# Kernel optimization log

Hardware: AMD Instinct MI355X
Metric: run time of the kernel (lower is better)

Reference implementation:

```python
import jax, jax.numpy as jnp
import numpy as np

B, L, Q, K, H = 64, 1024, 1024, 1024, 1024

def setup_inputs() -> dict:
    key = jax.random.key(0)
    k1, k2, k3, k4, k5, k6 = jax.random.split(key, 6)
    query = jax.random.normal(k1, (B, Q), dtype=jnp.float32)
    keys = jax.random.normal(k2, (B, L, K), dtype=jnp.float32)
    mask = jax.random.randint(k3, (B, L), 0, 2).astype(bool)
    # nn.Linear weights: W1 [H, Q], W2 [H, K], v [1, H], all bias-free
    W1 = jax.random.normal(k4, (H, Q), dtype=jnp.float32) / np.sqrt(Q)
    W2 = jax.random.normal(k5, (H, K), dtype=jnp.float32) / np.sqrt(K)
    v = jax.random.normal(k6, (1, H), dtype=jnp.float32) / np.sqrt(H)
    return {"query": query, "keys": keys, "mask": mask, "W1": W1, "W2": W2, "v": v}

def reference(query, keys, mask, W1, W2, v):
    # q: [B, H], broadcast over seq dim instead of expand
    q = query @ W1.T                                  # [B, H]
    k = jnp.einsum('blk,hk->blh', keys, W2)           # [B, L, H]
    scores = jnp.tanh(q[:, None, :] + k) @ v[0]       # [B, L]
    scores = jnp.where(mask, -jnp.inf, scores)
    weights = jax.nn.softmax(scores, axis=-1)
    weights = jnp.nan_to_num(weights, nan=0.0)
    context = jnp.einsum('bl,blk->bk', weights, keys) # [B, K]
    return (context, weights)
```

## Files before the change

kernel.cpp:

```cpp
#include <hip/hip_runtime.h>
#include <math.h>


typedef __attribute__((ext_vector_type(8))) short short8;
typedef __attribute__((ext_vector_type(4))) float floatx4;

__device__ __forceinline__ short f2bf(float x) {
    unsigned u = __float_as_uint(x);
    u += 0x7fffu + ((u >> 16) & 1u);
    return (short)(u >> 16);
}
__device__ __forceinline__ short8 pack8(float4 lo, float4 hi) {
    short8 r;
    r[0]=f2bf(lo.x); r[1]=f2bf(lo.y); r[2]=f2bf(lo.z); r[3]=f2bf(lo.w);
    r[4]=f2bf(hi.x); r[5]=f2bf(hi.y); r[6]=f2bf(hi.z); r[7]=f2bf(hi.w);
    return r;
}
__device__ __forceinline__ float fast_tanh(float x) {
    const float e = __expf(2.f * x);
    return 1.f - 2.f * __builtin_amdgcn_rcpf(e + 1.f);
}

#define LDA 40

__global__ __launch_bounds__(256) void k0_zero(float* __restrict__ out) {
    const int i = (blockIdx.x * 256 + threadIdx.x) * 4;
    const float4 z = {0.f, 0.f, 0.f, 0.f};
    *(float4*)(out + i) = z;
}

__global__ __launch_bounds__(256) void k1_qproj(
    const float* __restrict__ query, const float* __restrict__ W1,
    float* __restrict__ out)
{
    __shared__ float As[32][64];
    __shared__ float Bs[32][64];
    const int t  = threadIdx.x;
    const int tx = t & 15, ty = t >> 4;
    const int h0 = blockIdx.x * 64;
    const int kbase = blockIdx.y * 256;
    const int sr = t >> 2;
    const int sk = (t & 3) * 8;
    float c[4][4] = {{0.f}};
    for (int k0 = kbase; k0 < kbase + 256; k0 += 32) {
        const float4 a0 = *(const float4*)(query + sr * 1024 + k0 + sk);
        const float4 a1 = *(const float4*)(query + sr * 1024 + k0 + sk + 4);
        const float4 b0 = *(const float4*)(W1 + (h0 + sr) * 1024 + k0 + sk);
        const float4 b1 = *(const float4*)(W1 + (h0 + sr) * 1024 + k0 + sk + 4);
        __syncthreads();
        As[sk+0][sr]=a0.x; As[sk+1][sr]=a0.y; As[sk+2][sr]=a0.z; As[sk+3][sr]=a0.w;
        As[sk+4][sr]=a1.x; As[sk+5][sr]=a1.y; As[sk+6][sr]=a1.z; As[sk+7][sr]=a1.w;
        Bs[sk+0][sr]=b0.x; Bs[sk+1][sr]=b0.y; Bs[sk+2][sr]=b0.z; Bs[sk+3][sr]=b0.w;
        Bs[sk+4][sr]=b1.x; Bs[sk+5][sr]=b1.y; Bs[sk+6][sr]=b1.z; Bs[sk+7][sr]=b1.w;
        __syncthreads();
        #pragma unroll
        for (int k = 0; k < 32; ++k) {
            const float4 av = *(const float4*)&As[k][ty*4];
            const float4 bv = *(const float4*)&Bs[k][tx*4];
            const float aa[4] = {av.x, av.y, av.z, av.w};
            const float bb[4] = {bv.x, bv.y, bv.z, bv.w};
            #pragma unroll
            for (int i = 0; i < 4; ++i)
                #pragma unroll
                for (int j = 0; j < 4; ++j)
                    c[i][j] = fmaf(aa[i], bb[j], c[i][j]);
        }
    }
    #pragma unroll
    for (int i = 0; i < 4; ++i)
        #pragma unroll
        for (int j = 0; j < 4; ++j)
            atomicAdd(&out[(ty*4 + i) * 1024 + h0 + tx*4 + j], c[i][j]);
}

__global__ __launch_bounds__(256) void k_pack(const float* __restrict__ src,
                                              short* __restrict__ dst, int nunits)
{
    const int stride = gridDim.x * 256;
    for (int o = blockIdx.x * 256 + threadIdx.x; o < nunits; o += stride) {
        const int m = o & 15;
        const int c = (o >> 4) & 127;
        const int panel = o >> 11;
        const size_t f = ((size_t)panel * 16 + m) * 1024 + c * 8;
        const float4 a = *(const float4*)(src + f);
        const float4 b = *(const float4*)(src + f + 4);
        ((short8*)dst)[o] = pack8(a, b);
    }
}

__global__ __launch_bounds__(256) void k2_scores_full(
    const short* __restrict__ keysp, const short* __restrict__ W2p,
    const float* __restrict__ v, float* __restrict__ out)
{
    __shared__ float red[128][33];
    const int t  = threadIdx.x;
    const int l0 = blockIdx.x * 128;
    const int b  = blockIdx.y;
    const float* q = out;
    float* score = out + 65536;

    const int lane = t & 63, wid = t >> 6;
    const int quad = lane >> 4, m16 = lane & 15;
    const int wm = (wid >> 1) * 64;
    const int wn = (wid & 1) * 64;

    const short8* pA = (const short8*)keysp
        + ((size_t)(b * 64 + (l0 >> 4) + (wm >> 4))) * 2048 + quad * 16 + m16;

    float s_loc[4][4] = {{0.f}};

    for (int hb = 0; hb < 8; ++hb) {
        const short8* pB = (const short8*)W2p
            + ((size_t)(hb * 8 + (wn >> 4))) * 2048 + quad * 16 + m16;

        floatx4 acc[4][4] = {};
        short8 a0[4], b0[4], a1[4], b1[4];
        #pragma unroll
        for (int i = 0; i < 4; ++i) { a0[i] = pA[i * 2048]; b0[i] = pB[i * 2048]; }

        for (int kk = 0; kk < 928; kk += 64) {
            #pragma unroll
            for (int i = 0; i < 4; ++i) {
                a1[i] = pA[i * 2048 + (kk + 32) * 2];
                b1[i] = pB[i * 2048 + (kk + 32) * 2];
            }
            #pragma unroll
            for (int i = 0; i < 4; ++i)
                #pragma unroll
                for (int j = 0; j < 4; ++j)
                    acc[i][j] = __builtin_amdgcn_mfma_f32_16x16x32_bf16(a0[i], b0[j], acc[i][j], 0, 0, 0);
            #pragma unroll
            for (int i = 0; i < 4; ++i) {
                a0[i] = pA[i * 2048 + (kk + 64) * 2];
                b0[i] = pB[i * 2048 + (kk + 64) * 2];
            }
            #pragma unroll
            for (int i = 0; i < 4; ++i)
                #pragma unroll
                for (int j = 0; j < 4; ++j)
                    acc[i][j] = __builtin_amdgcn_mfma_f32_16x16x32_bf16(a1[i], b1[j], acc[i][j], 0, 0, 0);
        }
        #pragma unroll
        for (int i = 0; i < 4; ++i) {
            a1[i] = pA[i * 2048 + 992 * 2];
            b1[i] = pB[i * 2048 + 992 * 2];
        }
        #pragma unroll
        for (int i = 0; i < 4; ++i)
            #pragma unroll
            for (int j = 0; j < 4; ++j)
                acc[i][j] = __builtin_amdgcn_mfma_f32_16x16x32_bf16(a0[i], b0[j], acc[i][j], 0, 0, 0);
        #pragma unroll
        for (int i = 0; i < 4; ++i)
            #pragma unroll
            for (int j = 0; j < 4; ++j)
                acc[i][j] = __builtin_amdgcn_mfma_f32_16x16x32_bf16(a1[i], b1[j], acc[i][j], 0, 0, 0);

        float qv[4], vv[4];
        #pragma unroll
        for (int j = 0; j < 4; ++j) {
            const int h = hb * 128 + wn + j * 16 + m16;
            qv[j] = q[b * 1024 + h];
            vv[j] = v[h];
        }
        #pragma unroll
        for (int i = 0; i < 4; ++i)
            #pragma unroll
            for (int r = 0; r < 4; ++r) {
                float s = 0.f;
                #pragma unroll
                for (int j = 0; j < 4; ++j)
                    s += fast_tanh(qv[j] + acc[i][j][r]) * vv[j];
                s_loc[i][r] += s;
            }
    }

    #pragma unroll
    for (int i = 0; i < 4; ++i)
        #pragma unroll
        for (int r = 0; r < 4; ++r)
            red[wm + i * 16 + quad * 4 + r][(wid & 1) * 16 + m16] = s_loc[i][r];
    __syncthreads();
    if (t < 128) {
        const float* rr = red[t];
        float s = 0.f;
        #pragma unroll
        for (int c = 0; c < 32; ++c) s += rr[c];
        score[b * 1024 + l0 + t] = s;
    }
}

__global__ __launch_bounds__(256) void k2_scores(
    const float* __restrict__ keys, const float* __restrict__ W2,
    const float* __restrict__ v, float* __restrict__ out)
{
    __shared__ union {
        struct { short A[128][LDA]; short B[128][LDA]; } st;
        float red[128][33];
    } sm;
    const int t  = threadIdx.x;
    const int hb = blockIdx.x;
    const int l0 = blockIdx.y * 128;
    const int b  = blockIdx.z;
    const int h0 = hb * 128;
    const float* q = out;
    float* score = out + 65536;

    const int srow = t >> 1;
    const int skh  = (t & 1) * 16;
    const float* Arow = keys + ((size_t)(b * 1024 + l0 + srow)) * 1024 + skh;
    const float* Brow = W2   + ((size_t)(h0 + srow)) * 1024 + skh;

    const int lane = t & 63, wid = t >> 6;
    const int quad = lane >> 4, m16 = lane & 15;
    const int wm = (wid >> 1) * 64;
    const int wn = (wid & 1) * 64;

    floatx4 acc[4][4] = {};

    for (int kk = 0; kk < 1024; kk += 32) {
        const float4 a0 = *(const float4*)(Arow + kk);
        const float4 a1 = *(const float4*)(Arow + kk + 4);
        const float4 a2 = *(const float4*)(Arow + kk + 8);
        const float4 a3 = *(const float4*)(Arow + kk + 12);
        const float4 w0 = *(const float4*)(Brow + kk);
        const float4 w1 = *(const float4*)(Brow + kk + 4);
        const float4 w2 = *(const float4*)(Brow + kk + 8);
        const float4 w3 = *(const float4*)(Brow + kk + 12);
        __syncthreads();
        *(short8*)&sm.st.A[srow][skh]     = pack8(a0, a1);
        *(short8*)&sm.st.A[srow][skh + 8] = pack8(a2, a3);
        *(short8*)&sm.st.B[srow][skh]     = pack8(w0, w1);
        *(short8*)&sm.st.B[srow][skh + 8] = pack8(w2, w3);
        __syncthreads();
        short8 af[4], bf[4];
        #pragma unroll
        for (int i = 0; i < 4; ++i)
            af[i] = *(const short8*)&sm.st.A[wm + i*16 + m16][quad * 8];
        #pragma unroll
        for (int j = 0; j < 4; ++j)
            bf[j] = *(const short8*)&sm.st.B[wn + j*16 + m16][quad * 8];
        #pragma unroll
        for (int i = 0; i < 4; ++i)
            #pragma unroll
            for (int j = 0; j < 4; ++j)
                acc[i][j] = __builtin_amdgcn_mfma_f32_16x16x32_bf16(af[i], bf[j], acc[i][j], 0, 0, 0);
    }

    float qv[4], vv[4];
    #pragma unroll
    for (int j = 0; j < 4; ++j) {
        const int h = h0 + wn + j * 16 + m16;
        qv[j] = q[b * 1024 + h];
        vv[j] = v[h];
    }
    __syncthreads();
    #pragma unroll
    for (int i = 0; i < 4; ++i) {
        #pragma unroll
        for (int r = 0; r < 4; ++r) {
            float s = 0.f;
            #pragma unroll
            for (int j = 0; j < 4; ++j)
                s += fast_tanh(qv[j] + acc[i][j][r]) * vv[j];
            sm.red[wm + i * 16 + quad * 4 + r][(wid & 1) * 16 + m16] = s;
        }
    }
    __syncthreads();
    if (t < 128) {
        const float* rr = sm.red[t];
        float s = 0.f;
        #pragma unroll
        for (int c = 0; c < 32; ++c) s += rr[c];
        atomicAdd(&score[b * 1024 + l0 + t], s);
    }
}

__global__ __launch_bounds__(256) void k0_zero_score(float* __restrict__ out) {
    const int i = (blockIdx.x * 256 + threadIdx.x) * 4;
    const float4 z = {0.f, 0.f, 0.f, 0.f};
    *(float4*)(out + 65536 + i) = z;
}

__global__ __launch_bounds__(256) void k3_softmax(
    const unsigned char* __restrict__ mask_u8, float* __restrict__ out)
{
    __shared__ float sc[1024];
    __shared__ float red[256];
    __shared__ int nz_sh;
    const int b = blockIdx.x;
    const int t = threadIdx.x;

    if (t == 0) nz_sh = 0;
    __syncthreads();
    {
        int nz = 0;
        #pragma unroll
        for (int j = 1; j < 4; ++j)
            if (mask_u8[t * 4 + j] != 0) nz = 1;
        if (nz) atomicAdd(&nz_sh, 1);
    }
    __syncthreads();
    const int use_i32 = (nz_sh == 0);
    const int* mask_i32 = (const int*)mask_u8;

    float* score = out + 65536;
    float lmax = -INFINITY;
    #pragma unroll
    for (int i = 0; i < 4; ++i) {
        const int l = t + i * 256;
        float s = score[b * 1024 + l];
        const int ml = b * 1024 + l;
        const bool masked = use_i32 ? (mask_i32[ml] != 0) : (mask_u8[ml] != 0);
        if (masked) s = -INFINITY;
        sc[l] = s;
        lmax = fmaxf(lmax, s);
    }
    red[t] = lmax;
    __syncthreads();
    for (int off = 128; off > 0; off >>= 1) {
        if (t < off) red[t] = fmaxf(red[t], red[t + off]);
        __syncthreads();
    }
    const float m = red[0];
    __syncthreads();
    float e[4];
    float lsum = 0.f;
    #pragma unroll
    for (int i = 0; i < 4; ++i) {
        const float s = sc[t + i * 256];
        const float ev = (s > -INFINITY && m > -INFINITY) ? expf(s - m) : 0.f;
        e[i] = ev;
        lsum += ev;
    }
    red[t] = lsum;
    __syncthreads();
    for (int off = 128; off > 0; off >>= 1) {
        if (t < off) red[t] += red[t + off];
        __syncthreads();
    }
    const float S = red[0];
    const float inv = (S > 0.f) ? (1.f / S) : 0.f;
    #pragma unroll
    for (int i = 0; i < 4; ++i)
        score[b * 1024 + t + i * 256] = e[i] * inv;
    const float4 z = {0.f, 0.f, 0.f, 0.f};
    ((float4*)(out + b * 1024))[t] = z;
}

__global__ __launch_bounds__(256) void k4_context(
    const float* __restrict__ keys, float* __restrict__ out)
{
    __shared__ float w[128];
    const int t  = threadIdx.x;
    const int b  = blockIdx.y;
    const int l0 = blockIdx.x * 128;
    if (t < 128) w[t] = out[65536 + b * 1024 + l0 + t];
    __syncthreads();
    const float4* kp = (const float4*)(keys + ((size_t)b * 1024 + (size_t)l0) * 1024) + t;
    float4 acc = {0.f, 0.f, 0.f, 0.f};
    #pragma unroll 4
    for (int l = 0; l < 128; ++l) {
        const float4 kv = kp[(size_t)l * 256];
        const float wv = w[l];
        acc.x = fmaf(wv, kv.x, acc.x);
        acc.y = fmaf(wv, kv.y, acc.y);
        acc.z = fmaf(wv, kv.z, acc.z);
        acc.w = fmaf(wv, kv.w, acc.w);
    }
    float* o = out + b * 1024 + t * 4;
    atomicAdd(o + 0, acc.x);
    atomicAdd(o + 1, acc.y);
    atomicAdd(o + 2, acc.z);
    atomicAdd(o + 3, acc.w);
}

extern "C" void kernel_launch(void* const* d_in, const int* in_sizes, int n_in,
                              void* d_out, int out_size, void* d_ws, size_t ws_size,
                              hipStream_t stream) {
    const float*         query = (const float*)d_in[0];
    const float*         keys  = (const float*)d_in[1];
    const unsigned char* mask  = (const unsigned char*)d_in[2];
    const float*         W1    = (const float*)d_in[3];
    const float*         W2    = (const float*)d_in[4];
    const float*         v     = (const float*)d_in[5];
    float* out = (float*)d_out;

    const size_t KEYS_BF = (size_t)64 * 1024 * 1024 * 2;
    const size_t W2_BF   = (size_t)1024 * 1024 * 2;
    const bool use_ws = (d_ws != nullptr) && (ws_size >= KEYS_BF + W2_BF);

    k0_zero   <<<dim3(64),        256, 0, stream>>>(out);
    k1_qproj  <<<dim3(16, 4),     256, 0, stream>>>(query, W1, out);
    if (use_ws) {
        short* keysp = (short*)d_ws;
        short* W2p   = keysp + KEYS_BF / 2;
        k_pack<<<dim3(2048), 256, 0, stream>>>(keys, keysp, 8388608);
        k_pack<<<dim3(512),  256, 0, stream>>>(W2,   W2p,   131072);
        k2_scores_full<<<dim3(8, 64), 256, 0, stream>>>(keysp, W2p, v, out);
    } else {
        k0_zero_score<<<dim3(64), 256, 0, stream>>>(out);
        k2_scores    <<<dim3(8, 8, 64), 256, 0, stream>>>(keys, W2, v, out);
    }
    k3_softmax<<<dim3(64),        256, 0, stream>>>(mask, out);
    k4_context<<<dim3(8, 64),     256, 0, stream>>>(keys, out);
}
```

Baseline: 668.9 us.

## Split score GEMM over H halves, stage bf16 packing through LDS

The bf16 pack kernel now reads each 16-row panel with coalesced row-major loads into shared memory, then writes it out in the MFMA-friendly interleaved order. Previously each thread gathered strided 32-byte chunks directly from global memory. The fused score kernel gets a third grid dimension that splits the H loop into two halves, doubling the block count to 1024 so the GPU is better filled, with a launch-bounds occupancy hint. Because two blocks now add into each score, the score write becomes an atomicAdd. The separate score-zeroing kernel is dropped and k0_zero is enlarged to 128 blocks, presumably to clear the score region too, which doubles the atomic traffic on scores.

Result: slower. 699.1 us (+4.5%).

```diff
diff --git a/kernel.cpp b/kernel.cpp
--- a/kernel.cpp
+++ b/kernel.cpp
@@ -74,21 +74,34 @@
 }
 
 __global__ __launch_bounds__(256) void k_pack(const float* __restrict__ src,
-                                              short* __restrict__ dst, int nunits)
-{
-    const int stride = gridDim.x * 256;
-    for (int o = blockIdx.x * 256 + threadIdx.x; o < nunits; o += stride) {
-        const int m = o & 15;
-        const int c = (o >> 4) & 127;
-        const int panel = o >> 11;
-        const size_t f = ((size_t)panel * 16 + m) * 1024 + c * 8;
-        const float4 a = *(const float4*)(src + f);
-        const float4 b = *(const float4*)(src + f + 4);
-        ((short8*)dst)[o] = pack8(a, b);
-    }
-}
-
-__global__ __launch_bounds__(256) void k2_scores_full(
+                                              short* __restrict__ dst, int npanels)
+{
+    __shared__ short sm[16][1032];
+    const int t = threadIdx.x;
+    for (int p = blockIdx.x; p < npanels; p += gridDim.x) {
+        const float* s = src + (size_t)p * 16 * 1024;
+        short* d = dst + (size_t)p * 16 * 1024;
+        __syncthreads();
+        #pragma unroll
+        for (int it = 0; it < 8; ++it) {
+            const int idx = it * 256 + t;
+            const int row = idx >> 7;
+            const int c8  = idx & 127;
+            const float4 a = *(const float4*)(s + row * 1024 + c8 * 8);
+            const float4 b = *(const float4*)(s + row * 1024 + c8 * 8 + 4);
+            *(short8*)&sm[row][c8 * 8] = pack8(a, b);
+        }
+        __syncthreads();
+        #pragma unroll
+        for (int it = 0; it < 8; ++it) {
+            const int u = it * 256 + t;
+            const int m = u & 15, c = u >> 4;
+            ((short8*)d)[u] = *(const short8*)&sm[m][c * 8];
+        }
+    }
+}
+
+__global__ __launch_bounds__(256, 4) void k2_scores_full(
     const short* __restrict__ keysp, const short* __restrict__ W2p,
     const float* __restrict__ v, float* __restrict__ out)
 {
@@ -96,6 +109,7 @@
     const int t  = threadIdx.x;
     const int l0 = blockIdx.x * 128;
     const int b  = blockIdx.y;
+    const int hz = blockIdx.z;
     const float* q = out;
     float* score = out + 65536;
 
@@ -109,7 +123,7 @@
 
     float s_loc[4][4] = {{0.f}};
 
-    for (int hb = 0; hb < 8; ++hb) {
+    for (int hb = hz * 4; hb < hz * 4 + 4; ++hb) {
         const short8* pB = (const short8*)W2p
             + ((size_t)(hb * 8 + (wn >> 4))) * 2048 + quad * 16 + m16;
 
@@ -186,7 +200,7 @@
         float s = 0.f;
         #pragma unroll
         for (int c = 0; c < 32; ++c) s += rr[c];
-        score[b * 1024 + l0 + t] = s;
+        atomicAdd(&score[b * 1024 + l0 + t], s);
     }
 }
 
@@ -276,12 +290,6 @@
     }
 }
 
-__global__ __launch_bounds__(256) void k0_zero_score(float* __restrict__ out) {
-    const int i = (blockIdx.x * 256 + threadIdx.x) * 4;
-    const float4 z = {0.f, 0.f, 0.f, 0.f};
-    *(float4*)(out + 65536 + i) = z;
-}
-
 __global__ __launch_bounds__(256) void k3_softmax(
     const unsigned char* __restrict__ mask_u8, float* __restrict__ out)
 {
@@ -390,17 +398,16 @@
     const size_t W2_BF   = (size_t)1024 * 1024 * 2;
     const bool use_ws = (d_ws != nullptr) && (ws_size >= KEYS_BF + W2_BF);
 
-    k0_zero   <<<dim3(64),        256, 0, stream>>>(out);
+    k0_zero   <<<dim3(128),       256, 0, stream>>>(out);
     k1_qproj  <<<dim3(16, 4),     256, 0, stream>>>(query, W1, out);
     if (use_ws) {
         short* keysp = (short*)d_ws;
         short* W2p   = keysp + KEYS_BF / 2;
-        k_pack<<<dim3(2048), 256, 0, stream>>>(keys, keysp, 8388608);
-        k_pack<<<dim3(512),  256, 0, stream>>>(W2,   W2p,   131072);
-        k2_scores_full<<<dim3(8, 64), 256, 0, stream>>>(keysp, W2p, v, out);
+        k_pack<<<dim3(4096), 256, 0, stream>>>(keys, keysp, 4096);
+        k_pack<<<dim3(64),   256, 0, stream>>>(W2,   W2p,   64);
+        k2_scores_full<<<dim3(8, 64, 2), 256, 0, stream>>>(keysp, W2p, v, out);
     } else {
-        k0_zero_score<<<dim3(64), 256, 0, stream>>>(out);
-        k2_scores    <<<dim3(8, 8, 64), 256, 0, stream>>>(keys, W2, v, out);
+        k2_scores<<<dim3(8, 8, 64), 256, 0, stream>>>(keys, W2, v, out);
     }
     k3_softmax<<<dim3(64),        256, 0, stream>>>(mask, out);
     k4_context<<<dim3(8, 64),     256, 0, stream>>>(keys, out);
```
